# Optimization experiments

Measured on AMD Instinct MI355X. Metric: run time of the kernel, lower is better.

Reference implementation:

```python
import jax, jax.numpy as jnp
import numpy as np


def setup_inputs() -> dict:
    key = jax.random.key(0)
    k1, k2, k3 = jax.random.split(key, 3)
    bs, seqlen, hidden = 2, 2048, 1024
    s, h = 4, 256  # sqrt_n_heads, head_size
    std = 0.02
    num_layers = 12
    hidden_states = jax.random.normal(k1, (bs, seqlen, hidden), dtype=jnp.float32)
    q_scale = 1.0 / np.sqrt(2.0 * num_layers * h)
    queries = jax.random.normal(k2, (s, h, h * s), dtype=jnp.float32) * std * q_scale
    combiners = jax.random.normal(k3, (s, h * s, h), dtype=jnp.float32) * (std * q_scale)
    return {"hidden_states": hidden_states, "queries": queries, "combiners": combiners}


def reference(hidden_states, queries, combiners):
    # queries: [s1, h, s*h], combiners: [s1, s*h, h]
    s, h, _ = queries.shape
    bs, S, E = hidden_states.shape
    x = hidden_states.reshape(bs, S, s, h)            # [b, t, s, h]
    qw = queries.reshape(s, h, s, h)                  # [s1, h_in, s2, h_out]
    # projected queries, already permuted to [s2, b, t, s1, f]
    Q = jnp.einsum('btae,aeqf->qbtaf', x, qw)
    # pre-attention scores: [s2, b, t, s1, u] (u = key position)  ~O(S^2)
    pre = jnp.einsum('qbtaf,buqf->qbtau', Q, x)
    # attention output, permuted to [s1, b, t, s2, g]
    attn = jnp.einsum('qbtau,buqg->abtqg', pre, x)
    attn = attn.reshape(s, bs, S, s * h)              # [s1, b, t, s2*h]
    out = jnp.einsum('abtk,akg->btag', attn, combiners)
    return out.reshape(bs, S, s * h)
```

## Files before the change

kernel.cpp:

```cpp
#include <hip/hip_runtime.h>
#include <hip/hip_bf16.h>


typedef unsigned short u16;
using short8  = __attribute__((ext_vector_type(8))) short;
using floatx4 = __attribute__((ext_vector_type(4))) float;

__device__ inline u16 f2bf(float f) {
    unsigned u = __float_as_uint(f);
    unsigned r = u + 0x7fffu + ((u >> 16) & 1u);
    return (u16)(r >> 16);
}

template <typename T>
__device__ inline void stage_row(const T* __restrict__ src, long ld,
                                 u16* __restrict__ dst, int tid) {
#pragma unroll
    for (int it = 0; it < 8; ++it) {
        const int flat = (it * 256 + tid) * 4;
        const int kl = flat & 63, rl = flat >> 6;
        ushort4 v;
        if (sizeof(T) == 4) {
            const float4 f = *(const float4*)&((const float*)src)[(long)rl * ld + kl];
            v.x = f2bf(f.x); v.y = f2bf(f.y); v.z = f2bf(f.z); v.w = f2bf(f.w);
        } else {
            v = *(const ushort4*)&((const u16*)src)[(long)rl * ld + kl];
        }
        const int chunk = ((kl >> 5) * 8 + (rl >> 4)) * 64 + ((kl >> 3) & 3) * 16 + (rl & 15);
        *(ushort4*)&dst[chunk * 8 + (kl & 7)] = v;
    }
}

template <typename TA, typename TB, bool ATOMIC>
__device__ inline void gemm_tile(const TA* __restrict__ A, long lda,
                                 const TB* __restrict__ B, long ldb,
                                 float* __restrict__ C, long ldc,
                                 int K, int m0, int n0) {
    __shared__ u16 As[8192];
    __shared__ u16 Bs[8192];
    const int tid = threadIdx.x, lane = tid & 63, w = tid >> 6;
    const int IA = (w & 1) * 4, JB = (w >> 1) * 4;
    floatx4 acc[4][4] = {};

    for (int k0 = 0; k0 < K; k0 += 64) {
        stage_row(A + k0, lda, As, tid);
        stage_row(B + k0, ldb, Bs, tid);
        __syncthreads();
#pragma unroll
        for (int s = 0; s < 2; ++s) {
            short8 af[4], bfr[4];
#pragma unroll
            for (int i = 0; i < 4; ++i)
                af[i] = *(const short8*)&As[((s * 8 + IA + i) * 64 + lane) * 8];
#pragma unroll
            for (int j = 0; j < 4; ++j)
                bfr[j] = *(const short8*)&Bs[((s * 8 + JB + j) * 64 + lane) * 8];
#pragma unroll
            for (int i = 0; i < 4; ++i)
#pragma unroll
                for (int j = 0; j < 4; ++j)
                    acc[i][j] = __builtin_amdgcn_mfma_f32_16x16x32_bf16(af[i], bfr[j], acc[i][j], 0, 0, 0);
        }
        __syncthreads();
    }
    const int rb = (lane >> 4) * 4, col = lane & 15;
#pragma unroll
    for (int i = 0; i < 4; ++i)
#pragma unroll
        for (int j = 0; j < 4; ++j)
#pragma unroll
            for (int r = 0; r < 4; ++r) {
                const int gm = m0 + IA * 16 + i * 16 + rb + r;
                const int gn = n0 + JB * 16 + j * 16 + col;
                float* p = &C[(long)gm * ldc + gn];
                if (ATOMIC) atomicAdd(p, acc[i][j][r]); else *p = acc[i][j][r];
            }
}

__device__ inline void transpose64(const float* __restrict__ src, long lds_,
                                   int r0, int c0,
                                   u16* __restrict__ dst, long ldd,
                                   float (*tile)[65], int t) {
#pragma unroll
    for (int it = 0; it < 4; ++it) {
        const int row = (t >> 4) + it * 16, cq = (t & 15) * 4;
        *(float4*)&tile[row][cq] = *(const float4*)&src[(long)(r0 + row) * lds_ + c0 + cq];
    }
    __syncthreads();
#pragma unroll
    for (int it = 0; it < 4; ++it) {
        const int cl = (t >> 4) + it * 16, rq = (t & 15) * 4;
        ushort4 v;
        v.x = f2bf(tile[rq + 0][cl]); v.y = f2bf(tile[rq + 1][cl]);
        v.z = f2bf(tile[rq + 2][cl]); v.w = f2bf(tile[rq + 3][cl]);
        *(ushort4*)&dst[(long)(c0 + cl) * ldd + r0 + rq] = v;
    }
}

__global__ __launch_bounds__(256) void k_prep(const float* __restrict__ x,
                                              const float* __restrict__ qw,
                                              const float* __restrict__ comb,
                                              u16* __restrict__ xb,
                                              u16* __restrict__ xt,
                                              u16* __restrict__ qb,
                                              u16* __restrict__ cb,
                                              float* __restrict__ GZ) {
    __shared__ float tile[64][65];
    const int bid = blockIdx.x, t = threadIdx.x;
    if (bid < 1024) {
        const int b = bid >> 9, local = bid & 511;
        const int u0 = (local & 31) * 64, f0 = (local >> 5) * 64;
        const float* src = x + (long)b * 2097152;
#pragma unroll
        for (int it = 0; it < 4; ++it) {
            const int row = (t >> 4) + it * 16, cq = (t & 15) * 4;
            const float4 f = *(const float4*)&src[(long)(u0 + row) * 1024 + f0 + cq];
            *(float4*)&tile[row][cq] = f;
            ushort4 v;
            v.x = f2bf(f.x); v.y = f2bf(f.y); v.z = f2bf(f.z); v.w = f2bf(f.w);
            *(ushort4*)&xb[(long)b * 2097152 + (long)(u0 + row) * 1024 + f0 + cq] = v;
        }
        __syncthreads();
#pragma unroll
        for (int it = 0; it < 4; ++it) {
            const int cl = (t >> 4) + it * 16, rq = (t & 15) * 4;
            ushort4 v;
            v.x = f2bf(tile[rq + 0][cl]); v.y = f2bf(tile[rq + 1][cl]);
            v.z = f2bf(tile[rq + 2][cl]); v.w = f2bf(tile[rq + 3][cl]);
            *(ushort4*)&xt[(long)b * 2097152 + (long)(f0 + cl) * 2048 + u0 + rq] = v;
        }
    } else if (bid < 1280) {
        const long base = (long)(bid - 1024) * 4096;
#pragma unroll
        for (int it = 0; it < 4; ++it) {
            const long off = base + (it * 256 + t) * 4;
            const float4 f = *(const float4*)&qw[off];
            ushort4 v;
            v.x = f2bf(f.x); v.y = f2bf(f.y); v.z = f2bf(f.z); v.w = f2bf(f.w);
            *(ushort4*)&qb[off] = v;
        }
    } else if (bid < 1536) {
        const int idx = bid - 1280, a = idx >> 6, local = idx & 63;
        const int k0 = (local & 15) * 64, g0 = (local >> 4) * 64;
        transpose64(comb + (long)a * 262144, 256, k0, g0,
                    cb + (long)a * 262144, 1024, tile, t);
    } else {
        float4 zero = {0.f, 0.f, 0.f, 0.f};
        float4* z = (float4*)GZ;
#pragma unroll
        for (int it = 0; it < 16; ++it)
            z[(long)(bid - 1536) * 4096 + it * 256 + t] = zero;
    }
}

__global__ __launch_bounds__(256) void k_gram(const u16* __restrict__ xt,
                                              float* __restrict__ G) {
    const int tile = blockIdx.x, bq = blockIdx.y, split = blockIdx.z;
    const int tm = tile >> 1, tn = tile & 1;
    const int b = bq >> 2, q = bq & 3;
    const u16* base = xt + (long)b * 2097152 + (long)q * 256 * 2048 + split * 256;
    gemm_tile<u16, u16, true>(base + (long)tm * 128 * 2048, 2048,
                              base + (long)tn * 128 * 2048, 2048,
                              G + (long)bq * 65536, 256,
                              256, tm * 128, tn * 128);
}

__global__ __launch_bounds__(256) void k_2a(const u16* __restrict__ cb,
                                            const float* __restrict__ G,
                                            float* __restrict__ Tt) {
    const int tile = blockIdx.x, i = blockIdx.y;
    const int tm = tile >> 1, tn = tile & 1;
    const int q = i & 3, ba = i >> 2, b = ba >> 2, a = ba & 3;
    gemm_tile<u16, float, false>(
        cb + (long)a * 262144 + (long)tm * 128 * 1024 + q * 256, 1024,
        G + (long)(b * 4 + q) * 65536 + (long)tn * 128 * 256, 256,
        Tt + (long)ba * 262144, 1024,
        256, tm * 128, q * 256 + tn * 128);
}

__global__ __launch_bounds__(256) void k_2b(const float* __restrict__ Tt,
                                            const u16* __restrict__ qb,
                                            float* __restrict__ Wt) {
    const int tile = blockIdx.x, ba = blockIdx.y, split = blockIdx.z;
    const int tm = tile >> 1, tn = tile & 1;
    const int a = ba & 3;
    gemm_tile<float, u16, true>(
        Tt + (long)ba * 262144 + (long)tm * 128 * 1024 + split * 256, 1024,
        qb + (long)a * 262144 + (long)tn * 128 * 1024 + split * 256, 1024,
        Wt + (long)ba * 65536, 256,
        256, tm * 128, tn * 128);
}

__global__ __launch_bounds__(256) void k_3(const u16* __restrict__ xb,
                                           const float* __restrict__ Wt,
                                           float* __restrict__ out) {
    const int tl = blockIdx.x, ba = blockIdx.y;
    const int tm = tl >> 1, tn = tl & 1;
    const int b = ba >> 2, a = ba & 3;
    gemm_tile<u16, float, false>(
        xb + (long)b * 2097152 + (long)tm * 128 * 1024 + a * 256, 1024,
        Wt + (long)ba * 65536 + (long)tn * 128 * 256, 256,
        out + (long)b * 2097152 + a * 256, 1024,
        256, tm * 128, tn * 128);
}

extern "C" void kernel_launch(void* const* d_in, const int* in_sizes, int n_in,
                              void* d_out, int out_size, void* d_ws, size_t ws_size,
                              hipStream_t stream) {
    const float* x    = (const float*)d_in[0];
    const float* qw   = (const float*)d_in[1];
    const float* comb = (const float*)d_in[2];
    float* out = (float*)d_out;

    char* ws = (char*)d_ws;
    float* G  = (float*)(ws);
    float* Wt = (float*)(ws + (2u << 20));
    float* Tt = (float*)(ws + (4u << 20));
    u16* xb   = (u16*)  (ws + (12u << 20));
    u16* xt   = (u16*)  (ws + (20u << 20));
    u16* qb   = (u16*)  (ws + (28u << 20));
    u16* cb   = (u16*)  (ws + (30u << 20));

    k_prep<<<1600, 256, 0, stream>>>(x, qw, comb, xb, xt, qb, cb, G);
    k_gram<<<dim3(4, 8, 8), 256, 0, stream>>>(xt, G);
    k_2a  <<<dim3(4, 32),   256, 0, stream>>>(cb, G, Tt);
    k_2b  <<<dim3(4, 8, 4), 256, 0, stream>>>(Tt, qb, Wt);
    k_3   <<<dim3(32, 8),   256, 0, stream>>>(xb, Wt, out);
}
```

Measured before the change: 141.8 us.

## Fuse five kernels into one persistent kernel with software grid barriers

```diff
diff --git a/kernel.cpp b/kernel.cpp
--- a/kernel.cpp
+++ b/kernel.cpp
@@ -35,9 +35,8 @@
 __device__ inline void gemm_tile(const TA* __restrict__ A, long lda,
                                  const TB* __restrict__ B, long ldb,
                                  float* __restrict__ C, long ldc,
-                                 int K, int m0, int n0) {
-    __shared__ u16 As[8192];
-    __shared__ u16 Bs[8192];
+                                 int K, int m0, int n0,
+                                 u16* __restrict__ As, u16* __restrict__ Bs) {
     const int tid = threadIdx.x, lane = tid & 63, w = tid >> 6;
     const int IA = (w & 1) * 4, JB = (w >> 1) * 4;
     floatx4 acc[4][4] = {};
@@ -97,111 +96,132 @@
     }
 }
 
-__global__ __launch_bounds__(256) void k_prep(const float* __restrict__ x,
-                                              const float* __restrict__ qw,
-                                              const float* __restrict__ comb,
-                                              u16* __restrict__ xb,
-                                              u16* __restrict__ xt,
-                                              u16* __restrict__ qb,
-                                              u16* __restrict__ cb,
-                                              float* __restrict__ GZ) {
+__device__ inline void grid_barrier(unsigned* __restrict__ bar) {
+    __syncthreads();
+    if (threadIdx.x == 0) {
+        __threadfence();
+        const unsigned old = atomicAdd(bar, 1u);
+        const unsigned target = (old / 256u + 1u) * 256u;
+        while (__hip_atomic_load(bar, __ATOMIC_RELAXED,
+                                 __HIP_MEMORY_SCOPE_AGENT) < target)
+            __builtin_amdgcn_s_sleep(2);
+        __threadfence();
+    }
+    __syncthreads();
+}
+
+__global__ __launch_bounds__(256) void k_fused(const float* __restrict__ x,
+                                               const float* __restrict__ qw,
+                                               const float* __restrict__ comb,
+                                               float* __restrict__ out,
+                                               float* __restrict__ G,
+                                               float* __restrict__ Tt,
+                                               float* __restrict__ Wt,
+                                               u16* __restrict__ xb,
+                                               u16* __restrict__ xt,
+                                               u16* __restrict__ qb,
+                                               u16* __restrict__ cb,
+                                               unsigned* __restrict__ bar) {
+    __shared__ u16 As[8192];
+    __shared__ u16 Bs[8192];
     __shared__ float tile[64][65];
     const int bid = blockIdx.x, t = threadIdx.x;
-    if (bid < 1024) {
-        const int b = bid >> 9, local = bid & 511;
-        const int u0 = (local & 31) * 64, f0 = (local >> 5) * 64;
-        const float* src = x + (long)b * 2097152;
-#pragma unroll
-        for (int it = 0; it < 4; ++it) {
-            const int row = (t >> 4) + it * 16, cq = (t & 15) * 4;
-            const float4 f = *(const float4*)&src[(long)(u0 + row) * 1024 + f0 + cq];
-            *(float4*)&tile[row][cq] = f;
-            ushort4 v;
-            v.x = f2bf(f.x); v.y = f2bf(f.y); v.z = f2bf(f.z); v.w = f2bf(f.w);
-            *(ushort4*)&xb[(long)b * 2097152 + (long)(u0 + row) * 1024 + f0 + cq] = v;
+
+    for (int j = bid; j < 1600; j += 256) {
+        if (j < 1024) {
+            const int b = j >> 9, local = j & 511;
+            const int u0 = (local & 31) * 64, f0 = (local >> 5) * 64;
+            const float* src = x + (long)b * 2097152;
+#pragma unroll
+            for (int it = 0; it < 4; ++it) {
+                const int row = (t >> 4) + it * 16, cq = (t & 15) * 4;
+                const float4 f = *(const float4*)&src[(long)(u0 + row) * 1024 + f0 + cq];
+                *(float4*)&tile[row][cq] = f;
+                ushort4 v;
+                v.x = f2bf(f.x); v.y = f2bf(f.y); v.z = f2bf(f.z); v.w = f2bf(f.w);
+                *(ushort4*)&xb[(long)b * 2097152 + (long)(u0 + row) * 1024 + f0 + cq] = v;
+            }
+            __syncthreads();
+#pragma unroll
+            for (int it = 0; it < 4; ++it) {
+                const int cl = (t >> 4) + it * 16, rq = (t & 15) * 4;
+                ushort4 v;
+                v.x = f2bf(tile[rq + 0][cl]); v.y = f2bf(tile[rq + 1][cl]);
+                v.z = f2bf(tile[rq + 2][cl]); v.w = f2bf(tile[rq + 3][cl]);
+                *(ushort4*)&xt[(long)b * 2097152 + (long)(f0 + cl) * 2048 + u0 + rq] = v;
+            }
+        } else if (j < 1280) {
+            const long base = (long)(j - 1024) * 4096;
+#pragma unroll
+            for (int it = 0; it < 4; ++it) {
+                const long off = base + (it * 256 + t) * 4;
+                const float4 f = *(const float4*)&qw[off];
+                ushort4 v;
+                v.x = f2bf(f.x); v.y = f2bf(f.y); v.z = f2bf(f.z); v.w = f2bf(f.w);
+                *(ushort4*)&qb[off] = v;
+            }
+        } else if (j < 1536) {
+            const int idx = j - 1280, a = idx >> 6, local = idx & 63;
+            const int k0 = (local & 15) * 64, g0 = (local >> 4) * 64;
+            transpose64(comb + (long)a * 262144, 256, k0, g0,
+                        cb + (long)a * 262144, 1024, tile, t);
+        } else {
+            float4 zero = {0.f, 0.f, 0.f, 0.f};
+            float4* z = (float4*)G;
+#pragma unroll
+            for (int it = 0; it < 16; ++it)
+                z[(long)(j - 1536) * 4096 + it * 256 + t] = zero;
         }
         __syncthreads();
-#pragma unroll
-        for (int it = 0; it < 4; ++it) {
-            const int cl = (t >> 4) + it * 16, rq = (t & 15) * 4;
-            ushort4 v;
-            v.x = f2bf(tile[rq + 0][cl]); v.y = f2bf(tile[rq + 1][cl]);
-            v.z = f2bf(tile[rq + 2][cl]); v.w = f2bf(tile[rq + 3][cl]);
-            *(ushort4*)&xt[(long)b * 2097152 + (long)(f0 + cl) * 2048 + u0 + rq] = v;
-        }
-    } else if (bid < 1280) {
-        const long base = (long)(bid - 1024) * 4096;
-#pragma unroll
-        for (int it = 0; it < 4; ++it) {
-            const long off = base + (it * 256 + t) * 4;
-            const float4 f = *(const float4*)&qw[off];
-            ushort4 v;
-            v.x = f2bf(f.x); v.y = f2bf(f.y); v.z = f2bf(f.z); v.w = f2bf(f.w);
-            *(ushort4*)&qb[off] = v;
-        }
-    } else if (bid < 1536) {
-        const int idx = bid - 1280, a = idx >> 6, local = idx & 63;
-        const int k0 = (local & 15) * 64, g0 = (local >> 4) * 64;
-        transpose64(comb + (long)a * 262144, 256, k0, g0,
-                    cb + (long)a * 262144, 1024, tile, t);
-    } else {
-        float4 zero = {0.f, 0.f, 0.f, 0.f};
-        float4* z = (float4*)GZ;
-#pragma unroll
-        for (int it = 0; it < 16; ++it)
-            z[(long)(bid - 1536) * 4096 + it * 256 + t] = zero;
-    }
-}
-
-__global__ __launch_bounds__(256) void k_gram(const u16* __restrict__ xt,
-                                              float* __restrict__ G) {
-    const int tile = blockIdx.x, bq = blockIdx.y, split = blockIdx.z;
-    const int tm = tile >> 1, tn = tile & 1;
-    const int b = bq >> 2, q = bq & 3;
-    const u16* base = xt + (long)b * 2097152 + (long)q * 256 * 2048 + split * 256;
-    gemm_tile<u16, u16, true>(base + (long)tm * 128 * 2048, 2048,
-                              base + (long)tn * 128 * 2048, 2048,
-                              G + (long)bq * 65536, 256,
-                              256, tm * 128, tn * 128);
-}
-
-__global__ __launch_bounds__(256) void k_2a(const u16* __restrict__ cb,
-                                            const float* __restrict__ G,
-                                            float* __restrict__ Tt) {
-    const int tile = blockIdx.x, i = blockIdx.y;
-    const int tm = tile >> 1, tn = tile & 1;
-    const int q = i & 3, ba = i >> 2, b = ba >> 2, a = ba & 3;
-    gemm_tile<u16, float, false>(
-        cb + (long)a * 262144 + (long)tm * 128 * 1024 + q * 256, 1024,
-        G + (long)(b * 4 + q) * 65536 + (long)tn * 128 * 256, 256,
-        Tt + (long)ba * 262144, 1024,
-        256, tm * 128, q * 256 + tn * 128);
-}
-
-__global__ __launch_bounds__(256) void k_2b(const float* __restrict__ Tt,
-                                            const u16* __restrict__ qb,
-                                            float* __restrict__ Wt) {
-    const int tile = blockIdx.x, ba = blockIdx.y, split = blockIdx.z;
-    const int tm = tile >> 1, tn = tile & 1;
-    const int a = ba & 3;
-    gemm_tile<float, u16, true>(
-        Tt + (long)ba * 262144 + (long)tm * 128 * 1024 + split * 256, 1024,
-        qb + (long)a * 262144 + (long)tn * 128 * 1024 + split * 256, 1024,
-        Wt + (long)ba * 65536, 256,
-        256, tm * 128, tn * 128);
-}
-
-__global__ __launch_bounds__(256) void k_3(const u16* __restrict__ xb,
-                                           const float* __restrict__ Wt,
-                                           float* __restrict__ out) {
-    const int tl = blockIdx.x, ba = blockIdx.y;
-    const int tm = tl >> 1, tn = tl & 1;
-    const int b = ba >> 2, a = ba & 3;
-    gemm_tile<u16, float, false>(
-        xb + (long)b * 2097152 + (long)tm * 128 * 1024 + a * 256, 1024,
-        Wt + (long)ba * 65536 + (long)tn * 128 * 256, 256,
-        out + (long)b * 2097152 + a * 256, 1024,
-        256, tm * 128, tn * 128);
+    }
+    grid_barrier(bar);
+
+    {
+        const int tl = bid & 3, bq = (bid >> 2) & 7, split = bid >> 5;
+        const int tm = tl >> 1, tn = tl & 1;
+        const int b = bq >> 2, q = bq & 3;
+        const u16* base = xt + (long)b * 2097152 + (long)q * 256 * 2048 + split * 256;
+        gemm_tile<u16, u16, true>(base + (long)tm * 128 * 2048, 2048,
+                                  base + (long)tn * 128 * 2048, 2048,
+                                  G + (long)bq * 65536, 256,
+                                  256, tm * 128, tn * 128, As, Bs);
+    }
+    grid_barrier(bar);
+
+    if (bid < 128) {
+        const int tl = bid & 3, i = bid >> 2;
+        const int tm = tl >> 1, tn = tl & 1;
+        const int q = i & 3, ba = i >> 2, b = ba >> 2, a = ba & 3;
+        gemm_tile<u16, float, false>(
+            cb + (long)a * 262144 + (long)tm * 128 * 1024 + q * 256, 1024,
+            G + (long)(b * 4 + q) * 65536 + (long)tn * 128 * 256, 256,
+            Tt + (long)ba * 262144, 1024,
+            256, tm * 128, q * 256 + tn * 128, As, Bs);
+    }
+    grid_barrier(bar);
+
+    if (bid < 128) {
+        const int tl = bid & 3, ba = (bid >> 2) & 7, split = bid >> 5;
+        const int tm = tl >> 1, tn = tl & 1;
+        const int a = ba & 3;
+        gemm_tile<float, u16, true>(
+            Tt + (long)ba * 262144 + (long)tm * 128 * 1024 + split * 256, 1024,
+            qb + (long)a * 262144 + (long)tn * 128 * 1024 + split * 256, 1024,
+            Wt + (long)ba * 65536, 256,
+            256, tm * 128, tn * 128, As, Bs);
+    }
+    grid_barrier(bar);
+
+    {
+        const int tl = bid & 31, ba = bid >> 5;
+        const int tm = tl >> 1, tn = tl & 1;
+        const int b = ba >> 2, a = ba & 3;
+        gemm_tile<u16, float, false>(
+            xb + (long)b * 2097152 + (long)tm * 128 * 1024 + a * 256, 1024,
+            Wt + (long)ba * 65536 + (long)tn * 128 * 256, 256,
+            out + (long)b * 2097152 + a * 256, 1024,
+            256, tm * 128, tn * 128, As, Bs);
+    }
 }
 
 extern "C" void kernel_launch(void* const* d_in, const int* in_sizes, int n_in,
@@ -220,10 +240,9 @@
     u16* xt   = (u16*)  (ws + (20u << 20));
     u16* qb   = (u16*)  (ws + (28u << 20));
     u16* cb   = (u16*)  (ws + (30u << 20));
-
-    k_prep<<<1600, 256, 0, stream>>>(x, qw, comb, xb, xt, qb, cb, G);
-    k_gram<<<dim3(4, 8, 8), 256, 0, stream>>>(xt, G);
-    k_2a  <<<dim3(4, 32),   256, 0, stream>>>(cb, G, Tt);
-    k_2b  <<<dim3(4, 8, 4), 256, 0, stream>>>(Tt, qb, Wt);
-    k_3   <<<dim3(32, 8),   256, 0, stream>>>(xb, Wt, out);
-}
+    unsigned* bar = (unsigned*)(ws + (32u << 20));
+
+    hipMemsetAsync(bar, 0, 64, stream);
+    k_fused<<<256, 256, 0, stream>>>(x, qw, comb, out, G, Tt, Wt,
+                                     xb, xt, qb, cb, bar);
+}
```

New measurement: 219.1 us. 54.6% more time.

## Shrink GEMM tiles to 64x64 and convert x and queries on the fly

Applied to the files above, without the earlier changes.

```diff
diff --git a/kernel.cpp b/kernel.cpp
--- a/kernel.cpp
+++ b/kernel.cpp
@@ -13,10 +13,10 @@
 }
 
 template <typename T>
-__device__ inline void stage_row(const T* __restrict__ src, long ld,
-                                 u16* __restrict__ dst, int tid) {
+__device__ inline void stage64(const T* __restrict__ src, long ld,
+                               u16* __restrict__ dst, int tid) {
 #pragma unroll
-    for (int it = 0; it < 8; ++it) {
+    for (int it = 0; it < 4; ++it) {
         const int flat = (it * 256 + tid) * 4;
         const int kl = flat & 63, rl = flat >> 6;
         ushort4 v;
@@ -26,7 +26,7 @@
         } else {
             v = *(const ushort4*)&((const u16*)src)[(long)rl * ld + kl];
         }
-        const int chunk = ((kl >> 5) * 8 + (rl >> 4)) * 64 + ((kl >> 3) & 3) * 16 + (rl & 15);
+        const int chunk = ((kl >> 5) * 4 + (rl >> 4)) * 64 + ((kl >> 3) & 3) * 16 + (rl & 15);
         *(ushort4*)&dst[chunk * 8 + (kl & 7)] = v;
     }
 }
@@ -36,42 +36,42 @@
                                  const TB* __restrict__ B, long ldb,
                                  float* __restrict__ C, long ldc,
                                  int K, int m0, int n0) {
-    __shared__ u16 As[8192];
-    __shared__ u16 Bs[8192];
+    __shared__ u16 As[4096];
+    __shared__ u16 Bs[4096];
     const int tid = threadIdx.x, lane = tid & 63, w = tid >> 6;
-    const int IA = (w & 1) * 4, JB = (w >> 1) * 4;
-    floatx4 acc[4][4] = {};
+    const int IA = (w & 1) * 2, JB = (w >> 1) * 2;
+    floatx4 acc[2][2] = {};
 
     for (int k0 = 0; k0 < K; k0 += 64) {
-        stage_row(A + k0, lda, As, tid);
-        stage_row(B + k0, ldb, Bs, tid);
+        stage64(A + k0, lda, As, tid);
+        stage64(B + k0, ldb, Bs, tid);
         __syncthreads();
 #pragma unroll
         for (int s = 0; s < 2; ++s) {
-            short8 af[4], bfr[4];
+            short8 af[2], bfr[2];
 #pragma unroll
-            for (int i = 0; i < 4; ++i)
-                af[i] = *(const short8*)&As[((s * 8 + IA + i) * 64 + lane) * 8];
+            for (int i = 0; i < 2; ++i)
+                af[i] = *(const short8*)&As[((s * 4 + IA + i) * 64 + lane) * 8];
 #pragma unroll
-            for (int j = 0; j < 4; ++j)
-                bfr[j] = *(const short8*)&Bs[((s * 8 + JB + j) * 64 + lane) * 8];
+            for (int j = 0; j < 2; ++j)
+                bfr[j] = *(const short8*)&Bs[((s * 4 + JB + j) * 64 + lane) * 8];
 #pragma unroll
-            for (int i = 0; i < 4; ++i)
+            for (int i = 0; i < 2; ++i)
 #pragma unroll
-                for (int j = 0; j < 4; ++j)
+                for (int j = 0; j < 2; ++j)
                     acc[i][j] = __builtin_amdgcn_mfma_f32_16x16x32_bf16(af[i], bfr[j], acc[i][j], 0, 0, 0);
         }
         __syncthreads();
     }
     const int rb = (lane >> 4) * 4, col = lane & 15;
 #pragma unroll
-    for (int i = 0; i < 4; ++i)
+    for (int i = 0; i < 2; ++i)
 #pragma unroll
-        for (int j = 0; j < 4; ++j)
+        for (int j = 0; j < 2; ++j)
 #pragma unroll
             for (int r = 0; r < 4; ++r) {
-                const int gm = m0 + IA * 16 + i * 16 + rb + r;
-                const int gn = n0 + JB * 16 + j * 16 + col;
+                const int gm = m0 + (IA + i) * 16 + rb + r;
+                const int gn = n0 + (JB + j) * 16 + col;
                 float* p = &C[(long)gm * ldc + gn];
                 if (ATOMIC) atomicAdd(p, acc[i][j][r]); else *p = acc[i][j][r];
             }
@@ -98,110 +98,81 @@
 }
 
 __global__ __launch_bounds__(256) void k_prep(const float* __restrict__ x,
-                                              const float* __restrict__ qw,
                                               const float* __restrict__ comb,
-                                              u16* __restrict__ xb,
                                               u16* __restrict__ xt,
-                                              u16* __restrict__ qb,
                                               u16* __restrict__ cb,
                                               float* __restrict__ GZ) {
     __shared__ float tile[64][65];
-    const int bid = blockIdx.x, t = threadIdx.x;
-    if (bid < 1024) {
-        const int b = bid >> 9, local = bid & 511;
+    const int j = blockIdx.x, t = threadIdx.x;
+    if (j < 1024) {
+        const int b = j >> 9, local = j & 511;
         const int u0 = (local & 31) * 64, f0 = (local >> 5) * 64;
-        const float* src = x + (long)b * 2097152;
-#pragma unroll
-        for (int it = 0; it < 4; ++it) {
-            const int row = (t >> 4) + it * 16, cq = (t & 15) * 4;
-            const float4 f = *(const float4*)&src[(long)(u0 + row) * 1024 + f0 + cq];
-            *(float4*)&tile[row][cq] = f;
-            ushort4 v;
-            v.x = f2bf(f.x); v.y = f2bf(f.y); v.z = f2bf(f.z); v.w = f2bf(f.w);
-            *(ushort4*)&xb[(long)b * 2097152 + (long)(u0 + row) * 1024 + f0 + cq] = v;
-        }
-        __syncthreads();
-#pragma unroll
-        for (int it = 0; it < 4; ++it) {
-            const int cl = (t >> 4) + it * 16, rq = (t & 15) * 4;
-            ushort4 v;
-            v.x = f2bf(tile[rq + 0][cl]); v.y = f2bf(tile[rq + 1][cl]);
-            v.z = f2bf(tile[rq + 2][cl]); v.w = f2bf(tile[rq + 3][cl]);
-            *(ushort4*)&xt[(long)b * 2097152 + (long)(f0 + cl) * 2048 + u0 + rq] = v;
-        }
-    } else if (bid < 1280) {
-        const long base = (long)(bid - 1024) * 4096;
-#pragma unroll
-        for (int it = 0; it < 4; ++it) {
-            const long off = base + (it * 256 + t) * 4;
-            const float4 f = *(const float4*)&qw[off];
-            ushort4 v;
-            v.x = f2bf(f.x); v.y = f2bf(f.y); v.z = f2bf(f.z); v.w = f2bf(f.w);
-            *(ushort4*)&qb[off] = v;
-        }
-    } else if (bid < 1536) {
-        const int idx = bid - 1280, a = idx >> 6, local = idx & 63;
+        transpose64(x + (long)b * 2097152, 1024, u0, f0,
+                    xt + (long)b * 2097152, 2048, tile, t);
+    } else if (j < 1280) {
+        const int idx = j - 1024, a = idx >> 6, local = idx & 63;
         const int k0 = (local & 15) * 64, g0 = (local >> 4) * 64;
         transpose64(comb + (long)a * 262144, 256, k0, g0,
                     cb + (long)a * 262144, 1024, tile, t);
     } else {
+        const int idx = j - 1280;
         float4 zero = {0.f, 0.f, 0.f, 0.f};
         float4* z = (float4*)GZ;
 #pragma unroll
-        for (int it = 0; it < 16; ++it)
-            z[(long)(bid - 1536) * 4096 + it * 256 + t] = zero;
+        for (int it = 0; it < 4; ++it)
+            z[(long)idx * 1024 + it * 256 + t] = zero;
     }
 }
 
 __global__ __launch_bounds__(256) void k_gram(const u16* __restrict__ xt,
                                               float* __restrict__ G) {
     const int tile = blockIdx.x, bq = blockIdx.y, split = blockIdx.z;
-    const int tm = tile >> 1, tn = tile & 1;
+    const int tm = tile >> 2, tn = tile & 3;
     const int b = bq >> 2, q = bq & 3;
     const u16* base = xt + (long)b * 2097152 + (long)q * 256 * 2048 + split * 256;
-    gemm_tile<u16, u16, true>(base + (long)tm * 128 * 2048, 2048,
-                              base + (long)tn * 128 * 2048, 2048,
+    gemm_tile<u16, u16, true>(base + (long)tm * 64 * 2048, 2048,
+                              base + (long)tn * 64 * 2048, 2048,
                               G + (long)bq * 65536, 256,
-                              256, tm * 128, tn * 128);
+                              256, tm * 64, tn * 64);
 }
 
 __global__ __launch_bounds__(256) void k_2a(const u16* __restrict__ cb,
                                             const float* __restrict__ G,
                                             float* __restrict__ Tt) {
     const int tile = blockIdx.x, i = blockIdx.y;
-    const int tm = tile >> 1, tn = tile & 1;
+    const int tm = tile >> 2, tn = tile & 3;
     const int q = i & 3, ba = i >> 2, b = ba >> 2, a = ba & 3;
     gemm_tile<u16, float, false>(
-        cb + (long)a * 262144 + (long)tm * 128 * 1024 + q * 256, 1024,
-        G + (long)(b * 4 + q) * 65536 + (long)tn * 128 * 256, 256,
+        cb + (long)a * 262144 + (long)tm * 64 * 1024 + q * 256, 1024,
+        G + (long)(b * 4 + q) * 65536 + (long)tn * 64 * 256, 256,
         Tt + (long)ba * 262144, 1024,
-        256, tm * 128, q * 256 + tn * 128);
+        256, tm * 64, q * 256 + tn * 64);
 }
 
 __global__ __launch_bounds__(256) void k_2b(const float* __restrict__ Tt,
-                                            const u16* __restrict__ qb,
+                                            const float* __restrict__ qw,
                                             float* __restrict__ Wt) {
     const int tile = blockIdx.x, ba = blockIdx.y, split = blockIdx.z;
-    const int tm = tile >> 1, tn = tile & 1;
+    const int tm = tile >> 2, tn = tile & 3;
     const int a = ba & 3;
-    gemm_tile<float, u16, true>(
-        Tt + (long)ba * 262144 + (long)tm * 128 * 1024 + split * 256, 1024,
-        qb + (long)a * 262144 + (long)tn * 128 * 1024 + split * 256, 1024,
+    gemm_tile<float, float, true>(
+        Tt + (long)ba * 262144 + (long)tm * 64 * 1024 + split * 256, 1024,
+        qw + (long)a * 262144 + (long)tn * 64 * 1024 + split * 256, 1024,
         Wt + (long)ba * 65536, 256,
-        256, tm * 128, tn * 128);
+        256, tm * 64, tn * 64);
 }
 
-__global__ __launch_bounds__(256) void k_3(const u16* __restrict__ xb,
+__global__ __launch_bounds__(256) void k_3(const float* __restrict__ x,
                                            const float* __restrict__ Wt,
                                            float* __restrict__ out) {
     const int tl = blockIdx.x, ba = blockIdx.y;
-    const int tm = tl >> 1, tn = tl & 1;
+    const int tm = tl >> 2, tn = tl & 3;
     const int b = ba >> 2, a = ba & 3;
-    gemm_tile<u16, float, false>(
-        xb + (long)b * 2097152 + (long)tm * 128 * 1024 + a * 256, 1024,
-        Wt + (long)ba * 65536 + (long)tn * 128 * 256, 256,
+    gemm_tile<float, float, false>(
+        x + (long)b * 2097152 + (long)tm * 64 * 1024 + a * 256, 1024,
+        Wt + (long)ba * 65536 + (long)tn * 64 * 256, 256,
         out + (long)b * 2097152 + a * 256, 1024,
-        256, tm * 128, tn * 128);
+        256, tm * 64, tn * 64);
 }
 
 extern "C" void kernel_launch(void* const* d_in, const int* in_sizes, int n_in,
@@ -216,14 +187,12 @@
     float* G  = (float*)(ws);
     float* Wt = (float*)(ws + (2u << 20));
     float* Tt = (float*)(ws + (4u << 20));
-    u16* xb   = (u16*)  (ws + (12u << 20));
-    u16* xt   = (u16*)  (ws + (20u << 20));
-    u16* qb   = (u16*)  (ws + (28u << 20));
-    u16* cb   = (u16*)  (ws + (30u << 20));
+    u16* xt   = (u16*)  (ws + (12u << 20));
+    u16* cb   = (u16*)  (ws + (20u << 20));
 
-    k_prep<<<1600, 256, 0, stream>>>(x, qw, comb, xb, xt, qb, cb, G);
-    k_gram<<<dim3(4, 8, 8), 256, 0, stream>>>(xt, G);
-    k_2a  <<<dim3(4, 32),   256, 0, stream>>>(cb, G, Tt);
-    k_2b  <<<dim3(4, 8, 4), 256, 0, stream>>>(Tt, qb, Wt);
-    k_3   <<<dim3(32, 8),   256, 0, stream>>>(xb, Wt, out);
+    k_prep<<<1536, 256, 0, stream>>>(x, comb, xt, cb, G);
+    k_gram<<<dim3(16, 8, 8), 256, 0, stream>>>(xt, G);
+    k_2a  <<<dim3(16, 32),   256, 0, stream>>>(cb, G, Tt);
+    k_2b  <<<dim3(16, 8, 4), 256, 0, stream>>>(Tt, qw, Wt);
+    k_3   <<<dim3(128, 8),   256, 0, stream>>>(x, Wt, out);
 }
```

After: 143.9 us. No clear change (+1.5%).
